# Optimization experiments

Measured on AMD Instinct MI355X. Metric: run time of the kernel, lower is better.

Reference implementation:

```python
import jax, jax.numpy as jnp
import numpy as np

A0 = 0.5291772105638411
KE = 14.399645351950548
KEHALF = KE / 2.0

def softplus_inverse(x):
    x = np.asarray(x, dtype=np.float64)
    return np.float32(x + np.log(-np.expm1(-x)))

def setup_inputs() -> dict:
    key = jax.random.key(0)
    k1, k2, k3, k4 = jax.random.split(key, 4)
    B, N, K = 16, 8192, 128
    neighbors = jax.random.randint(k1, (B, N, K), 0, N, dtype=jnp.int64)
    neighbor_mask = jnp.ones((B, N, K), dtype=jnp.float32)
    # atomic numbers in [1, 94] (Z=0 would break d/dp of Z**p)
    atomic_numbers = jax.random.randint(k2, (B, N), 0, 94, dtype=jnp.int64) + 1
    # distances scaled into a physical range [0.5, 5.5) Angstrom to avoid r->0
    distances = jax.random.uniform(k3, (B, N, K), dtype=jnp.float32) * 5.0 + 0.5
    p = lambda v: jnp.full((1,), softplus_inverse(v), dtype=jnp.float32)
    return {
        'neighbors': neighbors,
        'neighbor_mask': neighbor_mask,
        'atomic_numbers': atomic_numbers,
        'distances': distances,
        'adiv': p(1.0 / (0.8854 * A0)),
        'apow': p(0.23),
        'c1': p(0.1818), 'c2': p(0.5099), 'c3': p(0.2802), 'c4': p(0.02817),
        'a1': p(3.2), 'a2': p(0.9423), 'a3': p(0.4028), 'a4': p(0.2016),
    }

def reference(neighbors, neighbor_mask, atomic_numbers, distances,
              adiv, apow, c1, c2, c3, c4, a1, a2, a3, a4):
    sp = jax.nn.softplus
    Zf = atomic_numbers.astype(jnp.float32)            # [B, N]
    zpow = Zf ** sp(apow)                              # [B, N]
    # per-batch gather over neighbor index (sparse edge list, no NxN build)
    gather = jax.vmap(lambda v, nb: v[nb])             # ([N],[N,K]) -> [N,K]
    zpow_j = gather(zpow, neighbors)                   # [B, N, K]
    a = (zpow[:, :, None] + zpow_j) * sp(adiv) * neighbor_mask
    zizj = Zf[:, :, None] * gather(Zf, neighbors) * neighbor_mask
    c1s, c2s, c3s, c4s = sp(c1), sp(c2), sp(c3), sp(c4)
    csum = c1s + c2s + c3s + c4s
    f = (c1s / csum) * jnp.exp(-sp(a1) * a * distances) \
      + (c2s / csum) * jnp.exp(-sp(a2) * a * distances) \
      + (c3s / csum) * jnp.exp(-sp(a3) * a * distances) \
      + (c4s / csum) * jnp.exp(-sp(a4) * a * distances)
    corr = jnp.where(neighbor_mask != 0,
                     KEHALF * f * zizj / distances,
                     jnp.zeros_like(distances))        # [B, N, K]
    return jnp.sum(corr, axis=(-1, -2))[:, None]       # [B, 1]
```

## Files before the change

kernel.cpp:

```cpp
#include <hip/hip_runtime.h>


#define KEHALF_F 7.199822675975274f
#define LOG2E_F  1.4426950408889634f
#define DEPTH    4
#define GRAN     64
#define WPB      8
#define SLOTB    768

__device__ __forceinline__ float softplus_f(float x) {
    return (x > 20.f) ? x : log1pf(__expf(x));
}

__global__ void zbl_pre(const int* __restrict__ zn,
                        const float* __restrict__ adiv,
                        const float* __restrict__ apow,
                        const float* __restrict__ c1, const float* __restrict__ c2,
                        const float* __restrict__ c3, const float* __restrict__ c4,
                        const float* __restrict__ a1, const float* __restrict__ a2,
                        const float* __restrict__ a3, const float* __restrict__ a4,
                        unsigned short* __restrict__ packed, float* __restrict__ scal,
                        int total_atoms)
{
    int i = blockIdx.x * blockDim.x + threadIdx.x;
    const float spa = softplus_f(apow[0]);
    const float sad = softplus_f(adiv[0]);
    const float qb  = sad;
    const float qmax = sad * __expf(spa * __logf(94.f));
    const float qs  = (qmax - qb) * (1.f / 511.f);
    if (i == 0) {
        float s1 = softplus_f(c1[0]), s2 = softplus_f(c2[0]);
        float s3 = softplus_f(c3[0]), s4 = softplus_f(c4[0]);
        float inv = KEHALF_F / (s1 + s2 + s3 + s4);
        scal[0] = sad;
        scal[1] = s1 * inv;
        scal[2] = s2 * inv;
        scal[3] = s3 * inv;
        scal[4] = s4 * inv;
        scal[5] = -softplus_f(a1[0]) * LOG2E_F;
        scal[6] = -softplus_f(a2[0]) * LOG2E_F;
        scal[7] = -softplus_f(a3[0]) * LOG2E_F;
        scal[8] = -softplus_f(a4[0]) * LOG2E_F;
        scal[9]  = qb;
        scal[10] = qs;
    }
    if (i < total_atoms) {
        unsigned int Z = (unsigned int)zn[i];
        float Zf = (float)Z;
        float zps = sad * __expf(spa * __logf(Zf));
        float qf = (zps - qb) / qs;
        int q = (int)(qf + 0.5f);
        if (q < 0) q = 0;
        if (q > 511) q = 511;
        packed[i] = (unsigned short)(((unsigned)q << 7) | (Z & 0x7Fu));
    }
}

extern __shared__ unsigned short tab[];

#define STAGE(slotp, it) do {                                                     \
    const int off = (it) * GRAN + lane;                                           \
    __builtin_amdgcn_global_load_lds(                                             \
        (const __attribute__((address_space(1))) void*)(nb_ + off),               \
        (__attribute__((address_space(3))) void*)(slotp), 4, 0, 0);               \
    __builtin_amdgcn_global_load_lds(                                             \
        (const __attribute__((address_space(1))) void*)(mk_ + off),               \
        (__attribute__((address_space(3))) void*)((slotp) + 256), 4, 0, 0);       \
    __builtin_amdgcn_global_load_lds(                                             \
        (const __attribute__((address_space(1))) void*)(ds_ + off),               \
        (__attribute__((address_space(3))) void*)((slotp) + 512), 4, 0, 0);       \
} while (0)

#define CONSUME(sp, it) do {                                                      \
    const int   ji = *(const int*)  ((sp) + (lane << 2));                         \
    const float mm = *(const float*)((sp) + 256 + (lane << 2));                   \
    const float dd = *(const float*)((sp) + 512 + (lane << 2));                   \
    const int r = rw + ((it) << 6) + lane;                                        \
    const unsigned int wi_ = tab[r >> kshift];                                    \
    const unsigned int wj_ = tab[ji];                                             \
    const float zpi = fmaf((float)(wi_ >> 7), qs, qb);                            \
    const float Zi  = (float)(wi_ & 0x7Fu);                                       \
    const float zpj = fmaf((float)(wj_ >> 7), qs, qb);                            \
    const float Zj  = (float)(wj_ & 0x7Fu);                                       \
    const float zz = Zi * Zj * mm;                                                \
    const float ad = (zpi + zpj) * (mm * dd);                                     \
    const float f = w1 * exp2f(e1 * ad) + w2 * exp2f(e2 * ad)                     \
                  + w3 * exp2f(e3 * ad) + w4 * exp2f(e4 * ad);                    \
    const float gc = f * zz * __builtin_amdgcn_rcpf(dd);                          \
    acc += (mm != 0.f) ? gc : 0.f;                                                \
} while (0)

__global__ __launch_bounds__(512, 8) void zbl_main7(
        const int*            __restrict__ neighbors,
        const float*          __restrict__ mask,
        const float*          __restrict__ dist,
        const unsigned short* __restrict__ packed,
        const float*          __restrict__ scal,
        float*                __restrict__ out,
        int N, int kshift, int epb, int iters)
{
    __shared__ char stage[WPB][DEPTH][SLOTB];

    const int tid  = threadIdx.x;
    const int w    = tid >> 6;
    const int lane = tid & 63;
    const int b    = blockIdx.y;

    const int rw = (blockIdx.x * WPB + w) * (iters * GRAN);
    const size_t ebase = (size_t)b * epb + (size_t)rw;
    const int*   nb_ = neighbors + ebase;
    const float* mk_ = mask      + ebase;
    const float* ds_ = dist      + ebase;

    const uint4* s4 = (const uint4*)(packed + (size_t)b * N);
    const int n8 = N >> 3;
    uint4 tv0, tv1;
    const bool h0 = (tid < n8);
    const bool h1 = (tid + 512 < n8);
    if (h0) tv0 = s4[tid];
    if (h1) tv1 = s4[tid + 512];

    {
        char* sp0 = &stage[w][0][0];
        STAGE(sp0, 0);
        char* sp1 = &stage[w][1][0];
        STAGE(sp1, 1);
        char* sp2 = &stage[w][2][0];
        STAGE(sp2, 2);
        char* sp3 = &stage[w][3][0];
        STAGE(sp3, 3);
    }

    {
        uint4* t4 = (uint4*)tab;
        if (h0) t4[tid] = tv0;
        if (h1) t4[tid + 512] = tv1;
    }
    const float w1 = scal[1], w2 = scal[2], w3 = scal[3], w4 = scal[4];
    const float e1 = scal[5], e2 = scal[6], e3 = scal[7], e4 = scal[8];
    const float qb = scal[9], qs = scal[10];
    __syncthreads();

    float acc = 0.f;
    int it = 0;

    for (; it < iters - DEPTH; ++it) {
        asm volatile("s_waitcnt vmcnt(9)" ::: "memory");
        char* sp = &stage[w][it & (DEPTH - 1)][0];
        const int   ji = *(const int*)  (sp + (lane << 2));
        const float mm = *(const float*)(sp + 256 + (lane << 2));
        const float dd = *(const float*)(sp + 512 + (lane << 2));
        asm volatile("s_waitcnt lgkmcnt(0)" ::: "memory");
        STAGE(sp, it + DEPTH);
        const int r = rw + (it << 6) + lane;
        const unsigned int wi_ = tab[r >> kshift];
        const unsigned int wj_ = tab[ji];
        const float zpi = fmaf((float)(wi_ >> 7), qs, qb);
        const float Zi  = (float)(wi_ & 0x7Fu);
        const float zpj = fmaf((float)(wj_ >> 7), qs, qb);
        const float Zj  = (float)(wj_ & 0x7Fu);
        const float zz = Zi * Zj * mm;
        const float ad = (zpi + zpj) * (mm * dd);
        const float f = w1 * exp2f(e1 * ad) + w2 * exp2f(e2 * ad)
                      + w3 * exp2f(e3 * ad) + w4 * exp2f(e4 * ad);
        const float gc = f * zz * __builtin_amdgcn_rcpf(dd);
        acc += (mm != 0.f) ? gc : 0.f;
    }

    {
        asm volatile("s_waitcnt vmcnt(9)" ::: "memory");
        char* sp = &stage[w][it & (DEPTH - 1)][0];
        CONSUME(sp, it); ++it;
    }
    {
        asm volatile("s_waitcnt vmcnt(6)" ::: "memory");
        char* sp = &stage[w][it & (DEPTH - 1)][0];
        CONSUME(sp, it); ++it;
    }
    {
        asm volatile("s_waitcnt vmcnt(3)" ::: "memory");
        char* sp = &stage[w][it & (DEPTH - 1)][0];
        CONSUME(sp, it); ++it;
    }
    {
        asm volatile("s_waitcnt vmcnt(0)" ::: "memory");
        char* sp = &stage[w][it & (DEPTH - 1)][0];
        CONSUME(sp, it); ++it;
    }

    #pragma unroll
    for (int off = 32; off > 0; off >>= 1) acc += __shfl_down(acc, off);
    __syncthreads();
    float* wred = (float*)&stage[0][0][0];
    if (lane == 0) wred[w] = acc;
    __syncthreads();
    if (tid == 0) {
        float t = 0.f;
        #pragma unroll
        for (int i = 0; i < WPB; ++i) t += wred[i];
        atomicAdd(&out[b], t);
    }
}

__global__ void zbl_fallback(const int* __restrict__ neighbors,
                             const float* __restrict__ mask,
                             const float* __restrict__ dist,
                             const unsigned short* __restrict__ packed,
                             const float* __restrict__ scal,
                             float* __restrict__ out,
                             int N, int K, int epb, int total_edges)
{
    const int e = blockIdx.x * blockDim.x + threadIdx.x;
    if (e >= total_edges) return;
    const float w1 = scal[1], w2 = scal[2], w3 = scal[3], w4 = scal[4];
    const float e1 = scal[5], e2 = scal[6], e3 = scal[7], e4 = scal[8];
    const float qb = scal[9], qs = scal[10];
    const int b = e / epb;
    const int n = (e - b * epb) / K;
    const unsigned int wi = packed[(size_t)b * N + n];
    const unsigned int wj = packed[(size_t)b * N + neighbors[e]];
    const float zpi = fmaf((float)(wi >> 7), qs, qb);
    const float zpj = fmaf((float)(wj >> 7), qs, qb);
    const float Zi = (float)(wi & 0x7Fu), Zj = (float)(wj & 0x7Fu);
    const float m = mask[e], d = dist[e];
    const float a  = (zpi + zpj) * m;
    const float ad = a * d;
    const float f = w1 * exp2f(e1 * ad) + w2 * exp2f(e2 * ad)
                  + w3 * exp2f(e3 * ad) + w4 * exp2f(e4 * ad);
    const float corr = (m != 0.f) ? (f * Zi * Zj * m / d) : 0.f;
    if (corr != 0.f) atomicAdd(&out[b], corr);
}

extern "C" void kernel_launch(void* const* d_in, const int* in_sizes, int n_in,
                              void* d_out, int out_size, void* d_ws, size_t ws_size,
                              hipStream_t stream) {
    const int*   neighbors = (const int*)  d_in[0];
    const float* nb_mask   = (const float*)d_in[1];
    const int*   zn        = (const int*)  d_in[2];
    const float* dist      = (const float*)d_in[3];
    const float* adiv = (const float*)d_in[4];
    const float* apow = (const float*)d_in[5];
    const float* c1 = (const float*)d_in[6];
    const float* c2 = (const float*)d_in[7];
    const float* c3 = (const float*)d_in[8];
    const float* c4 = (const float*)d_in[9];
    const float* a1 = (const float*)d_in[10];
    const float* a2 = (const float*)d_in[11];
    const float* a3 = (const float*)d_in[12];
    const float* a4 = (const float*)d_in[13];

    const int total_edges = in_sizes[0];
    const int total_atoms = in_sizes[2];
    const int B = out_size;
    const int N = total_atoms / B;
    const int K = total_edges / total_atoms;
    const int epb = N * K;

    float*          scal   = (float*)d_ws;
    unsigned short* packed = (unsigned short*)((char*)d_ws + 64);

    hipMemsetAsync(d_out, 0, (size_t)out_size * sizeof(float), stream);

    {
        const int threads = 256;
        const int blocks = (total_atoms + threads - 1) / threads;
        zbl_pre<<<blocks, threads, 0, stream>>>(zn, adiv, apow, c1, c2, c3, c4,
                                                a1, a2, a3, a4,
                                                packed, scal, total_atoms);
    }

    int kshift = 0;
    while ((1 << kshift) < K && kshift < 30) kshift++;
    const bool kpow2 = ((1 << kshift) == K);

    const int ITERS = 32;
    const int span_block = WPB * GRAN * ITERS;
    const size_t lds_dyn = (size_t)N * 2;
    const bool fast = kpow2 && (N % 8 == 0) && (N <= 8192) &&
                      (epb % span_block == 0) &&
                      ((size_t)(64 + (size_t)total_atoms * 2) <= ws_size);
    if (fast) {
        const int bpb = epb / span_block;
        dim3 grid(bpb, B);
        zbl_main7<<<grid, 512, lds_dyn, stream>>>(
            neighbors, nb_mask, dist, packed, scal, (float*)d_out,
            N, kshift, epb, ITERS);
    } else {
        const int threads = 256;
        const int blocks = (total_edges + threads - 1) / threads;
        zbl_fallback<<<blocks, threads, 0, stream>>>(
            neighbors, nb_mask, dist, packed, scal, (float*)d_out,
            N, K, epb, total_edges);
    }
}
```

Baseline: 53.91 us.

## Stage edge data with single 16-byte LDS-direct loads and fold weights into exponent

Replaces the three per-lane 4-byte global-to-LDS loads per stage with one 16-byte load issued by 48 lanes covering neighbors, mask and distances, and retunes the vmcnt waits to one outstanding op per stage. Folds the mixing weights into the exp2 argument via precomputed log2 weights and drops the mask select, relying on the mask already zeroing the product. This cuts memory instruction count and ALU ops per edge, but it relies on 16-byte LDS-direct load support and on finite terms when the mask is zero.

Measured after the change: 51.75 us. 1.04x faster.

```diff
diff --git a/kernel.cpp b/kernel.cpp
--- a/kernel.cpp
+++ b/kernel.cpp
@@ -32,17 +32,19 @@
         float s1 = softplus_f(c1[0]), s2 = softplus_f(c2[0]);
         float s3 = softplus_f(c3[0]), s4 = softplus_f(c4[0]);
         float inv = KEHALF_F / (s1 + s2 + s3 + s4);
+        float w1 = s1 * inv, w2 = s2 * inv, w3 = s3 * inv, w4 = s4 * inv;
         scal[0] = sad;
-        scal[1] = s1 * inv;
-        scal[2] = s2 * inv;
-        scal[3] = s3 * inv;
-        scal[4] = s4 * inv;
+        scal[1] = w1; scal[2] = w2; scal[3] = w3; scal[4] = w4;
         scal[5] = -softplus_f(a1[0]) * LOG2E_F;
         scal[6] = -softplus_f(a2[0]) * LOG2E_F;
         scal[7] = -softplus_f(a3[0]) * LOG2E_F;
         scal[8] = -softplus_f(a4[0]) * LOG2E_F;
         scal[9]  = qb;
         scal[10] = qs;
+        scal[11] = __log2f(w1);
+        scal[12] = __log2f(w2);
+        scal[13] = __log2f(w3);
+        scal[14] = __log2f(w4);
     }
     if (i < total_atoms) {
         unsigned int Z = (unsigned int)zn[i];
@@ -58,17 +60,15 @@
 
 extern __shared__ unsigned short tab[];
 
-#define STAGE(slotp, it) do {                                                     \
-    const int off = (it) * GRAN + lane;                                           \
-    __builtin_amdgcn_global_load_lds(                                             \
-        (const __attribute__((address_space(1))) void*)(nb_ + off),               \
-        (__attribute__((address_space(3))) void*)(slotp), 4, 0, 0);               \
-    __builtin_amdgcn_global_load_lds(                                             \
-        (const __attribute__((address_space(1))) void*)(mk_ + off),               \
-        (__attribute__((address_space(3))) void*)((slotp) + 256), 4, 0, 0);       \
-    __builtin_amdgcn_global_load_lds(                                             \
-        (const __attribute__((address_space(1))) void*)(ds_ + off),               \
-        (__attribute__((address_space(3))) void*)((slotp) + 512), 4, 0, 0);       \
+#define STAGE1(slotp, it) do {                                                    \
+    const char* _g = (lane < 16) ? (const char*)(nb_ + ((it) << 6))               \
+                   : (lane < 32) ? (const char*)(mk_ + ((it) << 6))               \
+                                 : (const char*)(ds_ + ((it) << 6));              \
+    _g += (lane & 15) * 16;                                                       \
+    if (lane < 48)                                                                \
+        __builtin_amdgcn_global_load_lds(                                         \
+            (const __attribute__((address_space(1))) void*)_g,                    \
+            (__attribute__((address_space(3))) void*)(slotp), 16, 0, 0);          \
 } while (0)
 
 #define CONSUME(sp, it) do {                                                      \
@@ -84,13 +84,12 @@
     const float Zj  = (float)(wj_ & 0x7Fu);                                       \
     const float zz = Zi * Zj * mm;                                                \
     const float ad = (zpi + zpj) * (mm * dd);                                     \
-    const float f = w1 * exp2f(e1 * ad) + w2 * exp2f(e2 * ad)                     \
-                  + w3 * exp2f(e3 * ad) + w4 * exp2f(e4 * ad);                    \
-    const float gc = f * zz * __builtin_amdgcn_rcpf(dd);                          \
-    acc += (mm != 0.f) ? gc : 0.f;                                                \
+    const float f = exp2f(fmaf(e1, ad, l1)) + exp2f(fmaf(e2, ad, l2))             \
+                  + exp2f(fmaf(e3, ad, l3)) + exp2f(fmaf(e4, ad, l4));            \
+    acc += f * zz * __builtin_amdgcn_rcpf(dd);                                    \
 } while (0)
 
-__global__ __launch_bounds__(512, 8) void zbl_main7(
+__global__ __launch_bounds__(512, 8) void zbl_main8(
         const int*            __restrict__ neighbors,
         const float*          __restrict__ mask,
         const float*          __restrict__ dist,
@@ -121,14 +120,10 @@
     if (h1) tv1 = s4[tid + 512];
 
     {
-        char* sp0 = &stage[w][0][0];
-        STAGE(sp0, 0);
-        char* sp1 = &stage[w][1][0];
-        STAGE(sp1, 1);
-        char* sp2 = &stage[w][2][0];
-        STAGE(sp2, 2);
-        char* sp3 = &stage[w][3][0];
-        STAGE(sp3, 3);
+        char* sp0 = &stage[w][0][0]; STAGE1(sp0, 0);
+        char* sp1 = &stage[w][1][0]; STAGE1(sp1, 1);
+        char* sp2 = &stage[w][2][0]; STAGE1(sp2, 2);
+        char* sp3 = &stage[w][3][0]; STAGE1(sp3, 3);
     }
 
     {
@@ -136,22 +131,22 @@
         if (h0) t4[tid] = tv0;
         if (h1) t4[tid + 512] = tv1;
     }
-    const float w1 = scal[1], w2 = scal[2], w3 = scal[3], w4 = scal[4];
-    const float e1 = scal[5], e2 = scal[6], e3 = scal[7], e4 = scal[8];
-    const float qb = scal[9], qs = scal[10];
+    const float e1 = scal[5],  e2 = scal[6],  e3 = scal[7],  e4 = scal[8];
+    const float qb = scal[9],  qs = scal[10];
+    const float l1 = scal[11], l2 = scal[12], l3 = scal[13], l4 = scal[14];
     __syncthreads();
 
     float acc = 0.f;
     int it = 0;
 
     for (; it < iters - DEPTH; ++it) {
-        asm volatile("s_waitcnt vmcnt(9)" ::: "memory");
+        asm volatile("s_waitcnt vmcnt(3)" ::: "memory");
         char* sp = &stage[w][it & (DEPTH - 1)][0];
         const int   ji = *(const int*)  (sp + (lane << 2));
         const float mm = *(const float*)(sp + 256 + (lane << 2));
         const float dd = *(const float*)(sp + 512 + (lane << 2));
         asm volatile("s_waitcnt lgkmcnt(0)" ::: "memory");
-        STAGE(sp, it + DEPTH);
+        STAGE1(sp, it + DEPTH);
         const int r = rw + (it << 6) + lane;
         const unsigned int wi_ = tab[r >> kshift];
         const unsigned int wj_ = tab[ji];
@@ -161,24 +156,23 @@
         const float Zj  = (float)(wj_ & 0x7Fu);
         const float zz = Zi * Zj * mm;
         const float ad = (zpi + zpj) * (mm * dd);
-        const float f = w1 * exp2f(e1 * ad) + w2 * exp2f(e2 * ad)
-                      + w3 * exp2f(e3 * ad) + w4 * exp2f(e4 * ad);
-        const float gc = f * zz * __builtin_amdgcn_rcpf(dd);
-        acc += (mm != 0.f) ? gc : 0.f;
-    }
-
-    {
-        asm volatile("s_waitcnt vmcnt(9)" ::: "memory");
-        char* sp = &stage[w][it & (DEPTH - 1)][0];
-        CONSUME(sp, it); ++it;
-    }
-    {
-        asm volatile("s_waitcnt vmcnt(6)" ::: "memory");
-        char* sp = &stage[w][it & (DEPTH - 1)][0];
-        CONSUME(sp, it); ++it;
-    }
+        const float f = exp2f(fmaf(e1, ad, l1)) + exp2f(fmaf(e2, ad, l2))
+                      + exp2f(fmaf(e3, ad, l3)) + exp2f(fmaf(e4, ad, l4));
+        acc += f * zz * __builtin_amdgcn_rcpf(dd);
+    }
+
     {
         asm volatile("s_waitcnt vmcnt(3)" ::: "memory");
+        char* sp = &stage[w][it & (DEPTH - 1)][0];
+        CONSUME(sp, it); ++it;
+    }
+    {
+        asm volatile("s_waitcnt vmcnt(2)" ::: "memory");
+        char* sp = &stage[w][it & (DEPTH - 1)][0];
+        CONSUME(sp, it); ++it;
+    }
+    {
+        asm volatile("s_waitcnt vmcnt(1)" ::: "memory");
         char* sp = &stage[w][it & (DEPTH - 1)][0];
         CONSUME(sp, it); ++it;
     }
@@ -282,7 +276,7 @@
     if (fast) {
         const int bpb = epb / span_block;
         dim3 grid(bpb, B);
-        zbl_main7<<<grid, 512, lds_dyn, stream>>>(
+        zbl_main8<<<grid, 512, lds_dyn, stream>>>(
             neighbors, nb_mask, dist, packed, scal, (float*)d_out,
             N, kshift, epb, ITERS);
     } else {
```
